# Kernel tuning notes

Measured on AMD Instinct MI355X. Metric: run time of the kernel, lower is better.

Reference implementation:

```python
import jax, jax.numpy as jnp
import numpy as np

B, N, D, H = 4, 4096, 1024, 16
HD = D // H


def setup_inputs() -> dict:
    key = jax.random.key(0)
    k_x, k_qkv, k_proj, k_b = jax.random.split(key, 4)
    x = jax.random.normal(k_x, (B, N, D), dtype=jnp.float32)
    # torch nn.Linear weights: (out_features, in_features)
    w_qkv = jax.random.normal(k_qkv, (3 * D, D), dtype=jnp.float32) * (D ** -0.5)
    w_proj = jax.random.normal(k_proj, (D, D), dtype=jnp.float32) * (D ** -0.5)
    b_proj = jax.random.normal(k_b, (D,), dtype=jnp.float32) * 0.01
    return {"x": x, "w_qkv": w_qkv, "w_proj": w_proj, "b_proj": b_proj}


def reference(x, w_qkv, w_proj, b_proj):
    b, n, d = x.shape
    # qkv projection (no bias, qkv_bias=False)
    qkv = x @ w_qkv.T                       # (b, n, 3d)
    qkv = qkv.reshape(b, n, 3, H, HD)
    q, k, v = qkv[:, :, 0], qkv[:, :, 1], qkv[:, :, 2]   # each (b, n, H, HD)
    # Faithful to source: q @ k.transpose(-2,-1) with q,k of shape (b,n,H,HD)
    # -> per-token (H,H) attention across heads, softmax over last (head) axis.
    scale = HD ** -0.5
    attn = jnp.einsum('bnhd,bngd->bnhg', q, k) * scale   # (b, n, H, H)
    attn = jax.nn.softmax(attn, axis=-1)
    o = jnp.einsum('bnhg,bngd->bnhd', attn, v)           # (b, n, H, HD)
    # source: transpose(1,2).reshape(b,n,d) (contiguous copy then reshape)
    o = jnp.swapaxes(o, 1, 2).reshape(b, n, d)
    return o @ w_proj.T + b_proj
```

## Files before the change

kernel.cpp:

```cpp
#include <hip/hip_runtime.h>
#include <hip/hip_bf16.h>
#include <cstdint>
#include <cstddef>

#define NB      4
#define NSEQ    4096
#define DM      1024
#define NTOK    16384
#define QKV_N   3072

typedef __attribute__((ext_vector_type(8))) short short8_t;
typedef __attribute__((ext_vector_type(4))) float f32x4;

static __device__ __forceinline__ unsigned short f2bf(float f) {
    unsigned u = __builtin_bit_cast(unsigned, f);
    u += 0x7fffu + ((u >> 16) & 1u);
    return (unsigned short)(u >> 16);
}

static __device__ __forceinline__ void async16(const void* g, void* l) {
    __builtin_amdgcn_global_load_lds(
        (const __attribute__((address_space(1))) void*)g,
        (__attribute__((address_space(3))) void*)l, 16, 0, 0);
}

__global__ void cvt_all(const float* __restrict__ x,
                        const float* __restrict__ wqkv,
                        const float* __restrict__ wproj,
                        unsigned short* __restrict__ xb,
                        unsigned short* __restrict__ wqkvb,
                        unsigned short* __restrict__ wprojb)
{
    int i = blockIdx.x * blockDim.x + threadIdx.x;
    const float* src; unsigned short* dst; int off;
    if (i < 4194304)      { src = x;     dst = xb;     off = i; }
    else if (i < 4980736) { src = wqkv;  dst = wqkvb;  off = i - 4194304; }
    else                  { src = wproj; dst = wprojb; off = i - 4980736; }
    float4 f = ((const float4*)src)[off];
    unsigned lo = (unsigned)f2bf(f.x) | ((unsigned)f2bf(f.y) << 16);
    unsigned hi = (unsigned)f2bf(f.z) | ((unsigned)f2bf(f.w) << 16);
    ((uint2*)dst)[off] = make_uint2(lo, hi);
}

template <bool BF16_OUT, bool BIAS>
__global__ __launch_bounds__(512, 2)
void gemm256(const unsigned short* __restrict__ A,
             const unsigned short* __restrict__ Bm,
             void* __restrict__ Cv,
             const float* __restrict__ bias,
             int M, int N, int K)
{
    __shared__ alignas(16) unsigned short As[2][16384];
    __shared__ alignas(16) unsigned short Bs[2][16384];

    const int t    = threadIdx.x;
    const int lane = t & 63;
    const int wave = t >> 6;
    const int quad = lane >> 4;
    const int r16  = lane & 15;
    const int wm   = wave >> 2;
    const int wn   = wave & 3;

    const int nwg = gridDim.x;
    const int swz = (blockIdx.x & 7) * (nwg >> 3) + (blockIdx.x >> 3);
    const int ntn = N >> 8;
    const int tm  = swz / ntn, tn = swz - tm * ntn;
    const int m0  = tm << 8, n0 = tn << 8;

    const int srow = t >> 3;
    const int schk = ((t & 7) ^ (srow & 7)) << 3;
    const unsigned short* gA = A  + (size_t)(m0 + srow) * K + schk;
    const unsigned short* gB = Bm + (size_t)(n0 + srow) * K + schk;
    unsigned short* const lA = &As[0][0] + t * 8;
    unsigned short* const lB = &Bs[0][0] + t * 8;

    const int NT = K >> 6;

#define STA(buf, kt, r) async16(gA + (size_t)(r) * 64 * K + (size_t)(kt) * 64, \
                                lA + (buf) * 16384 + (r) * 4096)
#define STB(buf, kt, r) async16(gB + (size_t)(r) * 64 * K + (size_t)(kt) * 64, \
                                lB + (buf) * 16384 + (r) * 4096)

    const int cs0 = ((quad    ) ^ (r16 & 7)) << 3;
    const int cs1 = ((quad ^ 4) ^ (r16 & 7)) << 3;
    const int aRow = wm * 128 + r16;
    const int bRow = wn * 64  + r16;

    f32x4 acc[8][4] = {};

    STA(0,0,0); STA(0,0,1); STA(0,0,2); STA(0,0,3);
    STB(0,0,0); STB(0,0,1); STB(0,0,2); STB(0,0,3);
    STA(1,1,0); STA(1,1,1); STA(1,1,2); STA(1,1,3);
    STB(1,1,0); STB(1,1,1); STB(1,1,2); STB(1,1,3);
    asm volatile("s_waitcnt vmcnt(8)" ::: "memory");
    __builtin_amdgcn_s_barrier();

#define RD_A(QR) _Pragma("unroll") for (int ii = 0; ii < 4; ++ii) {            \
        a[ii][0] = *(const short8_t*)(Ab + (aRow + (QR)*64 + ii*16) * 64 + cs0); \
        a[ii][1] = *(const short8_t*)(Ab + (aRow + (QR)*64 + ii*16) * 64 + cs1); }
#define RD_B(bb, QC) _Pragma("unroll") for (int jj = 0; jj < 2; ++jj) {        \
        bb[jj][0] = *(const short8_t*)(Bb + (bRow + (QC)*32 + jj*16) * 64 + cs0); \
        bb[jj][1] = *(const short8_t*)(Bb + (bRow + (QC)*32 + jj*16) * 64 + cs1); }
#define MM(QR, QC, bb) _Pragma("unroll") for (int s = 0; s < 2; ++s)           \
      _Pragma("unroll") for (int ii = 0; ii < 4; ++ii)                          \
        _Pragma("unroll") for (int jj = 0; jj < 2; ++jj)                        \
          acc[(QR)*4+ii][(QC)*2+jj] = __builtin_amdgcn_mfma_f32_16x16x32_bf16( \
              a[ii][s], bb[jj][s], acc[(QR)*4+ii][(QC)*2+jj], 0, 0, 0);
#define SYNC_PRE  __builtin_amdgcn_s_barrier();                                \
                  asm volatile("s_waitcnt lgkmcnt(0)" ::: "memory");           \
                  __builtin_amdgcn_sched_barrier(0);                           \
                  __builtin_amdgcn_s_setprio(1);
#define SYNC_POST __builtin_amdgcn_s_setprio(0);                               \
                  __builtin_amdgcn_s_barrier();                                \
                  asm volatile("" ::: "memory");

    for (int g = 0; g < NT; ++g) {
        const int cur = g & 1;
        const unsigned short* Ab = &As[cur][0];
        const unsigned short* Bb = &Bs[cur][0];
        const bool pf = (g + 2 < NT);
        short8_t a[4][2], b0[2][2], b1[2][2];

        RD_A(0) RD_B(b0, 0)
        SYNC_PRE
        MM(0, 0, b0)
        SYNC_POST

        RD_B(b1, 1)
        if (pf) { STA(cur, g+2, 0); STA(cur, g+2, 2); }
        SYNC_PRE
        MM(0, 1, b1)
        SYNC_POST

        RD_A(1)
        if (pf) { STB(cur, g+2, 0); STB(cur, g+2, 1); }
        SYNC_PRE
        MM(1, 0, b0)
        SYNC_POST

        if (pf) { STA(cur, g+2, 1); STA(cur, g+2, 3);
                  STB(cur, g+2, 2); STB(cur, g+2, 3); }
        __builtin_amdgcn_s_barrier();
        __builtin_amdgcn_s_setprio(1);
        MM(1, 1, b1)
        __builtin_amdgcn_s_setprio(0);
        if (pf)              asm volatile("s_waitcnt vmcnt(8)" ::: "memory");
        else if (g + 1 < NT) asm volatile("s_waitcnt vmcnt(0)" ::: "memory");
        __builtin_amdgcn_s_barrier();
        asm volatile("" ::: "memory");
    }

#undef STA
#undef STB
#undef RD_A
#undef RD_B
#undef MM
#undef SYNC_PRE
#undef SYNC_POST

    #pragma unroll
    for (int ri = 0; ri < 8; ++ri) {
        const int row = m0 + wm * 128 + (ri >> 2) * 64 + (ri & 3) * 16 + quad * 4;
        #pragma unroll
        for (int cj = 0; cj < 4; ++cj) {
            const int col = n0 + wn * 64 + (cj >> 1) * 32 + (cj & 1) * 16 + r16;
            float bv = 0.f;
            if constexpr (BIAS) bv = bias[col];
            #pragma unroll
            for (int r = 0; r < 4; ++r) {
                float v = acc[ri][cj][r] + bv;
                if constexpr (BF16_OUT)
                    ((unsigned short*)Cv)[(size_t)(row + r) * N + col] = f2bf(v);
                else
                    ((float*)Cv)[(size_t)(row + r) * N + col] = v;
            }
        }
    }
}

__global__ __launch_bounds__(256)
void attn_kernel(const unsigned short* __restrict__ qkv,
                 unsigned short* __restrict__ operm)
{
    __shared__ alignas(16) unsigned short s_qkv[4][QKV_N];
    __shared__ alignas(16) unsigned short s_p[4][256];
    __shared__ alignas(16) unsigned short s_o[4][16 * 72];
    const int t     = threadIdx.x;
    const int lane  = t & 63;
    const int wave  = t >> 6;
    const int quad  = lane >> 4;
    const int r16   = lane & 15;
    const int token = blockIdx.x * 4 + wave;

    {
        const unsigned short* src = qkv + (size_t)token * QKV_N;
        #pragma unroll
        for (int i = 0; i < 6; ++i)
            async16(src + i * 512 + lane * 8, &s_qkv[wave][i * 512 + lane * 8]);
    }
    __syncthreads();

    const unsigned short* q  = &s_qkv[wave][0];
    const unsigned short* kk = q + 1024;
    const unsigned short* vv = q + 2048;

    f32x4 s = {};
    #pragma unroll
    for (int c = 0; c < 64; c += 32) {
        short8_t aq = *(const short8_t*)(q  + r16 * 64 + c + quad * 8);
        short8_t bk = *(const short8_t*)(kk + r16 * 64 + c + quad * 8);
        s = __builtin_amdgcn_mfma_f32_16x16x32_bf16(aq, bk, s, 0, 0, 0);
    }

    #pragma unroll
    for (int r = 0; r < 4; ++r) {
        float x = s[r] * 0.125f;
        float m = x;
        #pragma unroll
        for (int o = 1; o < 16; o <<= 1) m = fmaxf(m, __shfl_xor(m, o));
        float e = __expf(x - m);
        float su = e;
        #pragma unroll
        for (int o = 1; o < 16; o <<= 1) su += __shfl_xor(su, o);
        s_p[wave][(quad * 4 + r) * 16 + r16] = f2bf(e * __builtin_amdgcn_rcpf(su));
    }
    __syncthreads();

    short8_t pa = {};
    if (quad < 2) pa = *(const short8_t*)(&s_p[wave][r16 * 16 + quad * 8]);

    f32x4 o[4];
    #pragma unroll
    for (int j = 0; j < 4; ++j) {
        short8_t vb = {};
        if (quad < 2) {
            #pragma unroll
            for (int e = 0; e < 8; ++e)
                vb[e] = (short)vv[(quad * 8 + e) * 64 + j * 16 + r16];
        }
        f32x4 z = {};
        o[j] = __builtin_amdgcn_mfma_f32_16x16x32_bf16(pa, vb, z, 0, 0, 0);
    }

    #pragma unroll
    for (int j = 0; j < 4; ++j)
        #pragma unroll
        for (int r = 0; r < 4; ++r)
            s_o[wave][(quad * 4 + r) * 72 + j * 16 + r16] = f2bf(o[j][r]);
    __syncthreads();

    const int b    = token >> 12;
    const int npos = token & 4095;
    const size_t base = (size_t)b * (NSEQ * DM)
                      + (size_t)(npos >> 4) * 1024
                      + (size_t)(npos & 15) * 64;
    #pragma unroll
    for (int c = lane; c < 128; c += 64) {
        const int h = c >> 3, part = c & 7;
        int4 val = *(const int4*)(&s_o[wave][h * 72 + part * 8]);
        *(int4*)(operm + base + (size_t)h * (256 * 1024) + part * 8) = val;
    }
}

extern "C" void kernel_launch(void* const* d_in, const int* in_sizes, int n_in,
                              void* d_out, int out_size, void* d_ws, size_t ws_size,
                              hipStream_t stream)
{
    const float* x      = (const float*)d_in[0];
    const float* w_qkv  = (const float*)d_in[1];
    const float* w_proj = (const float*)d_in[2];
    const float* b_proj = (const float*)d_in[3];
    float* out = (float*)d_out;

    unsigned short* xb     = (unsigned short*)d_ws;
    unsigned short* wqkvb  = xb     + (size_t)16777216;
    unsigned short* wprojb = wqkvb  + (size_t)3145728;
    unsigned short* qkvb   = wprojb + (size_t)1048576;
    unsigned short* opermb = qkvb   + (size_t)50331648;

    cvt_all<<<20480, 256, 0, stream>>>(x, w_qkv, w_proj, xb, wqkvb, wprojb);

    gemm256<true, false><<<768, 512, 0, stream>>>(xb, wqkvb, qkvb, nullptr,
                                                  NTOK, QKV_N, DM);

    attn_kernel<<<NTOK / 4, 256, 0, stream>>>(qkvb, opermb);

    gemm256<false, true><<<256, 512, 0, stream>>>(opermb, wprojb, out, b_proj,
                                                  NTOK, DM, DM);
}
```

Baseline: 302.1 us.

## Software-pipeline LDS fragment reads across GEMM MMA quadrants and k-tiles

Restructures the GEMM main loop so the LDS fragment reads for the next quadrant, and for the next k-tile's first quadrant, are issued before the current quadrant's MFMAs. It waits with partial lgkmcnt/vmcnt counts instead of full drains, and reorders the global-to-LDS prefetch issue. The aim is to hide LDS read latency behind matrix work. In exchange it uses more registers for the extra fragment buffers, and the hand-tuned wait counts carry a correctness risk.

Measured after the change: 319.1 us. 5.6% more time.

```diff
diff --git a/kernel.cpp b/kernel.cpp
--- a/kernel.cpp
+++ b/kernel.cpp
@@ -87,76 +87,86 @@
     const int bRow = wn * 64  + r16;
 
     f32x4 acc[8][4] = {};
+    short8_t aCur[4][2], aHi[4][2], bEv[2][2], bOd[2][2];
+
+#define RD_A(dst, base, QR) _Pragma("unroll") for (int ii = 0; ii < 4; ++ii) {  \
+        dst[ii][0] = *(const short8_t*)((base) + (aRow + (QR)*64 + ii*16) * 64 + cs0); \
+        dst[ii][1] = *(const short8_t*)((base) + (aRow + (QR)*64 + ii*16) * 64 + cs1); }
+#define RD_B(dst, base, QC) _Pragma("unroll") for (int jj = 0; jj < 2; ++jj) {  \
+        dst[jj][0] = *(const short8_t*)((base) + (bRow + (QC)*32 + jj*16) * 64 + cs0); \
+        dst[jj][1] = *(const short8_t*)((base) + (bRow + (QC)*32 + jj*16) * 64 + cs1); }
+#define MMQ(av, bv, QR, QC) _Pragma("unroll") for (int s = 0; s < 2; ++s)       \
+      _Pragma("unroll") for (int ii = 0; ii < 4; ++ii)                           \
+        _Pragma("unroll") for (int jj = 0; jj < 2; ++jj)                         \
+          acc[(QR)*4+ii][(QC)*2+jj] = __builtin_amdgcn_mfma_f32_16x16x32_bf16(  \
+              av[ii][s], bv[jj][s], acc[(QR)*4+ii][(QC)*2+jj], 0, 0, 0);
+#define BAR  __builtin_amdgcn_s_barrier(); asm volatile("" ::: "memory");
+#define WAITL(n) asm volatile("s_waitcnt lgkmcnt(" #n ")" ::: "memory");         \
+                 __builtin_amdgcn_sched_barrier(0);
+#define WAITV(n) asm volatile("s_waitcnt vmcnt(" #n ")" ::: "memory");           \
+                 __builtin_amdgcn_sched_barrier(0);
+#define SETP(n)  __builtin_amdgcn_s_setprio(n);
 
     STA(0,0,0); STA(0,0,1); STA(0,0,2); STA(0,0,3);
     STB(0,0,0); STB(0,0,1); STB(0,0,2); STB(0,0,3);
     STA(1,1,0); STA(1,1,1); STA(1,1,2); STA(1,1,3);
     STB(1,1,0); STB(1,1,1); STB(1,1,2); STB(1,1,3);
-    asm volatile("s_waitcnt vmcnt(8)" ::: "memory");
-    __builtin_amdgcn_s_barrier();
-
-#define RD_A(QR) _Pragma("unroll") for (int ii = 0; ii < 4; ++ii) {            \
-        a[ii][0] = *(const short8_t*)(Ab + (aRow + (QR)*64 + ii*16) * 64 + cs0); \
-        a[ii][1] = *(const short8_t*)(Ab + (aRow + (QR)*64 + ii*16) * 64 + cs1); }
-#define RD_B(bb, QC) _Pragma("unroll") for (int jj = 0; jj < 2; ++jj) {        \
-        bb[jj][0] = *(const short8_t*)(Bb + (bRow + (QC)*32 + jj*16) * 64 + cs0); \
-        bb[jj][1] = *(const short8_t*)(Bb + (bRow + (QC)*32 + jj*16) * 64 + cs1); }
-#define MM(QR, QC, bb) _Pragma("unroll") for (int s = 0; s < 2; ++s)           \
-      _Pragma("unroll") for (int ii = 0; ii < 4; ++ii)                          \
-        _Pragma("unroll") for (int jj = 0; jj < 2; ++jj)                        \
-          acc[(QR)*4+ii][(QC)*2+jj] = __builtin_amdgcn_mfma_f32_16x16x32_bf16( \
-              a[ii][s], bb[jj][s], acc[(QR)*4+ii][(QC)*2+jj], 0, 0, 0);
-#define SYNC_PRE  __builtin_amdgcn_s_barrier();                                \
-                  asm volatile("s_waitcnt lgkmcnt(0)" ::: "memory");           \
-                  __builtin_amdgcn_sched_barrier(0);                           \
-                  __builtin_amdgcn_s_setprio(1);
-#define SYNC_POST __builtin_amdgcn_s_setprio(0);                               \
-                  __builtin_amdgcn_s_barrier();                                \
-                  asm volatile("" ::: "memory");
+    WAITV(8)
+    BAR
+    RD_A(aCur, &As[0][0], 0)
+    RD_B(bEv,  &Bs[0][0], 0)
 
     for (int g = 0; g < NT; ++g) {
         const int cur = g & 1;
         const unsigned short* Ab = &As[cur][0];
         const unsigned short* Bb = &Bs[cur][0];
+        const unsigned short* An = &As[cur ^ 1][0];
+        const unsigned short* Bn = &Bs[cur ^ 1][0];
         const bool pf = (g + 2 < NT);
-        short8_t a[4][2], b0[2][2], b1[2][2];
-
-        RD_A(0) RD_B(b0, 0)
-        SYNC_PRE
-        MM(0, 0, b0)
-        SYNC_POST
-
-        RD_B(b1, 1)
+        const bool rn = (g + 1 < NT);
+
+        RD_B(bOd, Bb, 1)
+        BAR
+        WAITL(4)
+        SETP(1) MMQ(aCur, bEv, 0, 0) SETP(0)
+        BAR
+
         if (pf) { STA(cur, g+2, 0); STA(cur, g+2, 2); }
-        SYNC_PRE
-        MM(0, 1, b1)
-        SYNC_POST
-
-        RD_A(1)
-        if (pf) { STB(cur, g+2, 0); STB(cur, g+2, 1); }
-        SYNC_PRE
-        MM(1, 0, b0)
-        SYNC_POST
-
-        if (pf) { STA(cur, g+2, 1); STA(cur, g+2, 3);
+        RD_A(aHi, Ab, 1)
+        BAR
+        WAITL(8)
+        SETP(1) MMQ(aCur, bOd, 0, 1) SETP(0)
+        BAR
+
+        if (pf) { STB(cur, g+2, 0); STB(cur, g+2, 1);
                   STB(cur, g+2, 2); STB(cur, g+2, 3); }
-        __builtin_amdgcn_s_barrier();
-        __builtin_amdgcn_s_setprio(1);
-        MM(1, 1, b1)
-        __builtin_amdgcn_s_setprio(0);
-        if (pf)              asm volatile("s_waitcnt vmcnt(8)" ::: "memory");
-        else if (g + 1 < NT) asm volatile("s_waitcnt vmcnt(0)" ::: "memory");
-        __builtin_amdgcn_s_barrier();
-        asm volatile("" ::: "memory");
+        if (pf) { WAITV(6) } else { WAITV(0) }
+        BAR
+        if (rn) {
+            RD_A(aCur, An, 0)
+            WAITL(8)
+        } else {
+            WAITL(0)
+        }
+        SETP(1) MMQ(aHi, bEv, 1, 0) SETP(0)
+        BAR
+
+        if (pf) { STA(cur, g+2, 1); STA(cur, g+2, 3); }
+        if (rn) { RD_B(bEv, Bn, 0) }
+        BAR
+        SETP(1) MMQ(aHi, bOd, 1, 1) SETP(0)
+        BAR
     }
 
 #undef STA
 #undef STB
 #undef RD_A
 #undef RD_B
-#undef MM
-#undef SYNC_PRE
-#undef SYNC_POST
+#undef MMQ
+#undef BAR
+#undef WAITL
+#undef WAITV
+#undef SETP
 
     #pragma unroll
     for (int ri = 0; ri < 8; ++ri) {
```
